# Optimization experiments

Hardware: AMD Instinct MI355X
Metric: run time of the kernel (lower is better)

The kernel has to match this reference:

```python
import jax, jax.numpy as jnp
from jax import lax
import numpy as np

# Reconstructed utils constants
PSZ = 24     # patch size
KS = 3       # kernel size of generated conv kernels
FILTERS = 9  # channels / number of generated filters
STRIDE = 8   # conv stride inside KGL


def setup_inputs() -> dict:
    key = jax.random.key(0)
    k1, k2, k3 = jax.random.split(key, 3)
    B, H, W = 8, 768, 768
    x = jax.random.normal(k1, (B, H, W, FILTERS), dtype=jnp.float32)
    conv_w = jax.random.normal(k2, (KS, KS, FILTERS, 9), dtype=jnp.float32) * 0.05  # HWIO
    conv_b = jnp.zeros((9,), dtype=jnp.float32)
    dense_w = jax.random.normal(k3, (FILTERS, FILTERS * FILTERS), dtype=jnp.float32) * 0.05
    dense_b = jnp.zeros((FILTERS * FILTERS,), dtype=jnp.float32)
    return {"x": x, "conv_w": conv_w, "conv_b": conv_b, "dense_w": dense_w, "dense_b": dense_b}


def _clip_by_norm(t, axes, clip_norm=1.0):
    # tf.clip_by_norm: t * clip_norm / max(||t||_2_over_axes, clip_norm)
    l2 = jnp.sqrt(jnp.sum(t * t, axis=axes, keepdims=True))
    return t * (clip_norm / jnp.maximum(l2, clip_norm))


def reference(x, conv_w, conv_b, dense_w, dense_b):
    B, H, W, C = x.shape
    p1, p2 = H // PSZ, W // PSZ
    N = p1 * p2
    # tf.image.extract_patches layout: [B, p1, p2, PSZ*PSZ*C] with patch flattened row-major (row, col, chan)
    patches = x.reshape(B, p1, PSZ, p2, PSZ, C).transpose(0, 1, 3, 2, 4, 5)  # [B,p1,p2,PSZ,PSZ,C]
    # RAW reshape to (N, B, PSZ, PSZ, C) exactly as the TF code does (buffer reinterpretation)
    patches = patches.reshape(N, B, PSZ, PSZ, C)
    flat = patches.reshape(N * B, PSZ, PSZ, C)

    # --- W_G1: per-patch conv kernel generation ---
    conv_out = lax.conv_general_dilated(
        flat, conv_w, window_strides=(STRIDE, STRIDE), padding="SAME",
        dimension_numbers=("NHWC", "HWIO", "NHWC")) + conv_b  # [N*B, 3, 3, 9]
    wg1 = conv_out.reshape(N * B, KS, KS, FILTERS, 1)
    wg1 = _clip_by_norm(wg1, axes=(1, 2))                      # norm over (KS, KS) dims
    wg1 = wg1.reshape(N, B, KS, KS, FILTERS, 1)

    # --- W_G2: per-patch 1x1 mixing kernel via GAP + Dense ---
    gap = flat.mean(axis=(1, 2))                               # [N*B, C]
    d = gap @ dense_w + dense_b                                # [N*B, FILTERS^2]
    wg2 = d.reshape(N * B, 1, 1, FILTERS, FILTERS)
    wg2 = _clip_by_norm(wg2, axes=(1, 2, 3))
    wg2 = wg2.reshape(N, B, 1, 1, FILTERS, FILTERS)
    return wg1, wg2
```

## Files before the change

kernel.cpp:

```cpp
#include <hip/hip_runtime.h>


#define PSZ 24
#define NCH 9
#define HW 768
#define NPIX (PSZ*PSZ)
#define ROWF (PSZ*NCH)
#define ROWV4 54
#define XROWF (HW*NCH)
#define OUT2_OFF 663552

__global__ __launch_bounds__(256) void kgl_kernel(
    const float* __restrict__ x,
    const float* __restrict__ conv_w,
    const float* __restrict__ conv_b,
    const float* __restrict__ dense_w,
    const float* __restrict__ dense_b,
    float* __restrict__ out)
{
    __shared__ __align__(16) float cwA[732];
    __shared__ __align__(16) float cwB[732];
    __shared__ __align__(16) float colA[ROWF];
    __shared__ __align__(16) float colB[ROWF];
    __shared__ float gapA[NCH];
    __shared__ float gapB[NCH];
    __shared__ float co_s[81];
    __shared__ float d_s[81];

    const int j   = blockIdx.x;
    const int b   = j >> 10;
    const int rem = j & 1023;
    const int pi  = rem >> 5;
    const int pj  = rem & 31;
    const int tid = threadIdx.x;

    const size_t base = ((size_t)(b*HW + pi*PSZ) * HW + (size_t)pj*PSZ) * NCH;
    const float* gbase = x + base;

    float conv_acc = 0.f;

    if (tid < 128) {
        float* cw = (tid < 64) ? cwA : cwB;
        const int lane = tid & 63;
        #pragma unroll
        for (int i = 0; i < 3; ++i) {
            int e = lane + i*64;
            if (e < 182)
                reinterpret_cast<float4*>(cw)[e] =
                    reinterpret_cast<const float4*>(conv_w)[e];
        }
        if (lane == 0) cw[728] = conv_w[728];

        if (tid < 81) {
            const int oy = tid / 27;
            const int ox = (tid / 9) % 3;
            const int oc = tid % 9;
            float acc = conv_b[oc];
            #pragma unroll
            for (int ky = 0; ky < 3; ++ky) {
                const float* gp = gbase + (size_t)(oy*8+ky)*XROWF + (size_t)(ox*8)*NCH;
                const float4* gp4 = reinterpret_cast<const float4*>(gp);
                float pv[28];
                #pragma unroll
                for (int q = 0; q < 7; ++q) {
                    float4 v = gp4[q];
                    pv[q*4+0] = v.x; pv[q*4+1] = v.y; pv[q*4+2] = v.z; pv[q*4+3] = v.w;
                }
                #pragma unroll
                for (int kx = 0; kx < 3; ++kx) {
                    #pragma unroll
                    for (int ic = 0; ic < 9; ++ic)
                        acc += pv[kx*9+ic] * cw[(ky*3+kx)*81 + ic*9 + oc];
                }
            }
            co_s[tid] = acc;
            conv_acc = acc;
        }
    } else {
        const int w  = (tid >= 192) ? 1 : 0;
        const int k  = tid & 63;
        const int r0 = w ? 12 : 0;
        if (k < ROWV4) {
            float4 acc = make_float4(0.f, 0.f, 0.f, 0.f);
            #pragma unroll
            for (int r = 0; r < 12; ++r) {
                float4 v = *reinterpret_cast<const float4*>(
                    gbase + (size_t)(r0 + r)*XROWF + (size_t)k*4);
                acc.x += v.x; acc.y += v.y; acc.z += v.z; acc.w += v.w;
            }
            reinterpret_cast<float4*>(w ? colB : colA)[k] = acc;
        }
        if (k < NCH) {
            const float* col = w ? colB : colA;
            float s = 0.f;
            #pragma unroll
            for (int i = 0; i < 24; ++i) s += col[k + NCH*i];
            if (w) gapB[k] = s; else gapA[k] = s;
        }
    }
    __syncthreads();

    if (tid < 81) {
        const int oc = tid % 9;
        float n2 = 0.f;
        #pragma unroll
        for (int s = 0; s < 9; ++s) {
            float v = co_s[s*9 + oc];
            n2 += v*v;
        }
        float sc = 1.0f / fmaxf(sqrtf(n2), 1.0f);
        out[(size_t)j*81 + tid] = conv_acc * sc;

        float d = dense_b[tid];
        #pragma unroll
        for (int c = 0; c < NCH; ++c)
            d += (gapA[c] + gapB[c]) * (1.0f/(float)NPIX) * dense_w[c*81 + tid];
        d_s[tid] = d;
    }
    __syncthreads();

    if (tid < 81) {
        const int bc = tid % 9;
        float n2 = 0.f;
        #pragma unroll
        for (int a = 0; a < 9; ++a) {
            float v = d_s[a*9 + bc];
            n2 += v*v;
        }
        float sc = 1.0f / fmaxf(sqrtf(n2), 1.0f);
        out[OUT2_OFF + (size_t)j*81 + tid] = d_s[tid] * sc;
    }
}

extern "C" void kernel_launch(void* const* d_in, const int* in_sizes, int n_in,
                              void* d_out, int out_size, void* d_ws, size_t ws_size,
                              hipStream_t stream) {
    const float* x       = (const float*)d_in[0];
    const float* conv_w  = (const float*)d_in[1];
    const float* conv_b  = (const float*)d_in[2];
    const float* dense_w = (const float*)d_in[3];
    const float* dense_b = (const float*)d_in[4];
    float* out = (float*)d_out;

    kgl_kernel<<<8192, 256, 0, stream>>>(x, conv_w, conv_b, dense_w, dense_b, out);
}
```

Measured before the change: 238.9 us.

## Stage conv input rows in shared memory and spread GAP loads over all waves

All four waves now load six patch rows each for the GAP column sums. While doing so they copy the nine rows needed by the strided conv into shared memory. The conv threads then read their inputs from LDS instead of issuing separate global loads, so those rows are no longer fetched twice. The cost is an extra __syncthreads before the conv and a larger LDS footprint per block, which may reduce occupancy.

```diff
diff --git a/kernel.cpp b/kernel.cpp
--- a/kernel.cpp
+++ b/kernel.cpp
@@ -18,30 +18,26 @@
     const float* __restrict__ dense_b,
     float* __restrict__ out)
 {
-    __shared__ __align__(16) float cwA[732];
-    __shared__ __align__(16) float cwB[732];
-    __shared__ __align__(16) float colA[ROWF];
-    __shared__ __align__(16) float colB[ROWF];
-    __shared__ float gapA[NCH];
-    __shared__ float gapB[NCH];
+    __shared__ __align__(16) float convrows[9*ROWF];
+    __shared__ __align__(16) float cw[732];
+    __shared__ __align__(16) float colP[4*ROWF];
+    __shared__ float gap_s[NCH];
     __shared__ float co_s[81];
     __shared__ float d_s[81];
 
-    const int j   = blockIdx.x;
-    const int b   = j >> 10;
-    const int rem = j & 1023;
-    const int pi  = rem >> 5;
-    const int pj  = rem & 31;
-    const int tid = threadIdx.x;
+    const int j    = blockIdx.x;
+    const int b    = j >> 10;
+    const int rem  = j & 1023;
+    const int pi   = rem >> 5;
+    const int pj   = rem & 31;
+    const int tid  = threadIdx.x;
+    const int w    = tid >> 6;
+    const int lane = tid & 63;
 
     const size_t base = ((size_t)(b*HW + pi*PSZ) * HW + (size_t)pj*PSZ) * NCH;
     const float* gbase = x + base;
 
-    float conv_acc = 0.f;
-
-    if (tid < 128) {
-        float* cw = (tid < 64) ? cwA : cwB;
-        const int lane = tid & 63;
+    if (w == 0) {
         #pragma unroll
         for (int i = 0; i < 3; ++i) {
             int e = lane + i*64;
@@ -50,53 +46,57 @@
                     reinterpret_cast<const float4*>(conv_w)[e];
         }
         if (lane == 0) cw[728] = conv_w[728];
+    }
+    if (lane < ROWV4) {
+        float4 acc = make_float4(0.f, 0.f, 0.f, 0.f);
+        #pragma unroll
+        for (int r6 = 0; r6 < 6; ++r6) {
+            const int row = w*6 + r6;
+            float4 v = *reinterpret_cast<const float4*>(
+                gbase + (size_t)row*XROWF + (size_t)lane*4);
+            acc.x += v.x; acc.y += v.y; acc.z += v.z; acc.w += v.w;
+            if ((row & 7) < 3) {
+                const int ci = (row & 7) + 3*(row >> 3);
+                reinterpret_cast<float4*>(convrows)[ci*ROWV4 + lane] = v;
+            }
+        }
+        reinterpret_cast<float4*>(colP)[w*ROWV4 + lane] = acc;
+    }
+    __syncthreads();
 
-        if (tid < 81) {
-            const int oy = tid / 27;
-            const int ox = (tid / 9) % 3;
-            const int oc = tid % 9;
-            float acc = conv_b[oc];
+    float conv_acc = 0.f;
+    if (tid < 81) {
+        const int oy = tid / 27;
+        const int ox = (tid / 9) % 3;
+        const int oc = tid % 9;
+        float acc = conv_b[oc];
+        #pragma unroll
+        for (int ky = 0; ky < 3; ++ky) {
+            const float* rp = &convrows[(3*oy + ky)*ROWF + ox*72];
+            float pv[28];
             #pragma unroll
-            for (int ky = 0; ky < 3; ++ky) {
-                const float* gp = gbase + (size_t)(oy*8+ky)*XROWF + (size_t)(ox*8)*NCH;
-                const float4* gp4 = reinterpret_cast<const float4*>(gp);
-                float pv[28];
+            for (int q = 0; q < 7; ++q) {
+                float4 v = reinterpret_cast<const float4*>(rp)[q];
+                pv[q*4+0] = v.x; pv[q*4+1] = v.y; pv[q*4+2] = v.z; pv[q*4+3] = v.w;
+            }
+            #pragma unroll
+            for (int kx = 0; kx < 3; ++kx) {
                 #pragma unroll
-                for (int q = 0; q < 7; ++q) {
-                    float4 v = gp4[q];
-                    pv[q*4+0] = v.x; pv[q*4+1] = v.y; pv[q*4+2] = v.z; pv[q*4+3] = v.w;
-                }
-                #pragma unroll
-                for (int kx = 0; kx < 3; ++kx) {
-                    #pragma unroll
-                    for (int ic = 0; ic < 9; ++ic)
-                        acc += pv[kx*9+ic] * cw[(ky*3+kx)*81 + ic*9 + oc];
-                }
+                for (int ic = 0; ic < 9; ++ic)
+                    acc += pv[kx*9+ic] * cw[(ky*3+kx)*81 + ic*9 + oc];
             }
-            co_s[tid] = acc;
-            conv_acc = acc;
         }
-    } else {
-        const int w  = (tid >= 192) ? 1 : 0;
-        const int k  = tid & 63;
-        const int r0 = w ? 12 : 0;
-        if (k < ROWV4) {
-            float4 acc = make_float4(0.f, 0.f, 0.f, 0.f);
+        co_s[tid] = acc;
+        conv_acc = acc;
+    } else if (tid >= 128 && tid < 128 + NCH) {
+        const int c = tid - 128;
+        float s = 0.f;
+        #pragma unroll
+        for (int wv = 0; wv < 4; ++wv)
             #pragma unroll
-            for (int r = 0; r < 12; ++r) {
-                float4 v = *reinterpret_cast<const float4*>(
-                    gbase + (size_t)(r0 + r)*XROWF + (size_t)k*4);
-                acc.x += v.x; acc.y += v.y; acc.z += v.z; acc.w += v.w;
-            }
-            reinterpret_cast<float4*>(w ? colB : colA)[k] = acc;
-        }
-        if (k < NCH) {
-            const float* col = w ? colB : colA;
-            float s = 0.f;
-            #pragma unroll
-            for (int i = 0; i < 24; ++i) s += col[k + NCH*i];
-            if (w) gapB[k] = s; else gapA[k] = s;
-        }
+            for (int i = 0; i < 24; ++i)
+                s += colP[wv*ROWF + c + NCH*i];
+        gap_s[c] = s * (1.0f / (float)NPIX);
     }
     __syncthreads();
 
@@ -114,7 +114,7 @@
         float d = dense_b[tid];
         #pragma unroll
         for (int c = 0; c < NCH; ++c)
-            d += (gapA[c] + gapB[c]) * (1.0f/(float)NPIX) * dense_w[c*81 + tid];
+            d += gap_s[c] * dense_w[c*81 + tid];
         d_s[tid] = d;
     }
     __syncthreads();
```

After: 245.0 us. 2.6% more time.
